# Kernel optimization log

Hardware: AMD Instinct MI355X
Metric: run time of the kernel (lower is better)

The kernel has to match this reference:

```python
import jax, jax.numpy as jnp
import numpy as np

BS, NC, C, D = 8, 64, 256, 32
K, KB, ALPHA, B = 16, 8, 4, 16
HS, HM, HMOD = 64, 64, 32
N = NC * C
DLM = NC * D
MOD_IN = K + 3 * D + 1    # 113
MOD_OUT = K + KB + 1 + D  # 57


def setup_inputs() -> dict:
    key = jax.random.key(0)
    ks = jax.random.split(key, 12)
    rn = lambda k, s, sc=1.0: jax.random.normal(k, s, dtype=jnp.float32) * sc
    s_in, m_in = 3 * D + 1, 3 * D
    inp = {}
    inp['cc_signals_t'] = rn(ks[0], (BS, DLM))
    inp['h'] = rn(ks[1], (BS, NC, C, D), 0.1)
    inp['prev_messages'] = rn(ks[2], (BS, NC, C, D), 0.1)
    inp['decay_logit'] = jnp.zeros((BS, NC, C), jnp.float32)
    inp['primitives_state'] = jnp.zeros((BS, NC, C, D), jnp.float32)
    inp['hebbian_traces'] = jnp.zeros((BS, NC, C, K), jnp.float32)
    inp['state_w1'] = rn(ks[3], (HS, s_in), (2.0 / (s_in + HS)) ** 0.5)
    inp['state_b1'] = jnp.zeros((HS,), jnp.float32)
    inp['state_w2'] = rn(ks[4], (D, HS), (2.0 / (HS + D)) ** 0.5)
    inp['state_b2'] = jnp.zeros((D,), jnp.float32)
    inp['msg_w1'] = rn(ks[5], (HM, m_in), (2.0 / (m_in + HM)) ** 0.5)
    inp['msg_b1'] = jnp.zeros((HM,), jnp.float32)
    inp['msg_w2'] = rn(ks[6], (D, HM), (2.0 / (HM + D)) ** 0.5)
    inp['msg_b2'] = jnp.zeros((D,), jnp.float32)
    inp['mod_w1'] = rn(ks[7], (N, HMOD, MOD_IN), (2.0 / (MOD_IN + HMOD)) ** 0.5)
    inp['mod_b1'] = jnp.zeros((N, HMOD), jnp.float32)
    inp['mod_w2'] = rn(ks[8], (N, HMOD, MOD_OUT), (2.0 / (HMOD + MOD_OUT)) ** 0.5)
    inp['mod_b2'] = jnp.zeros((N, MOD_OUT), jnp.float32)
    inp['neuron_id'] = rn(ks[9], (NC, C, D), 1.0 / D ** 0.5)
    inp['conn_indices'] = jax.random.randint(ks[10], (NC, C, K), 0, C)
    inp['border_conn_indices'] = jax.random.randint(ks[11], (NC, B, KB), 0, NC * B)
    return inp


def reference(cc_signals_t, h, prev_messages, decay_logit, primitives_state,
              hebbian_traces, state_w1, state_b1, state_w2, state_b2,
              msg_w1, msg_b1, msg_w2, msg_b2,
              mod_w1, mod_b1, mod_w2, mod_b2, neuron_id,
              conn_indices, border_conn_indices):
    # ---- per-neuron modulator: each of N=NC*C neurons has unique MLP weights ----
    nid = jnp.broadcast_to(neuron_id[None], (BS, NC, C, D))
    mod_inp = jnp.concatenate(
        [hebbian_traces, h, decay_logit[..., None], primitives_state, nid], axis=-1)
    flat = mod_inp.reshape(BS, N, MOD_IN)
    hid = jnp.tanh(jnp.einsum('bni,nhi->bnh', flat, mod_w1) + mod_b1)
    out = (jnp.einsum('bnh,nho->bno', hid, mod_w2) + mod_b2).reshape(BS, NC, C, MOD_OUT)
    new_w_conn = out[..., :K]                          # [BS,NC,C,K]
    w_border = out[:, :, ALPHA:ALPHA + B, K:K + KB]    # border neurons only [BS,NC,B,KB]
    new_decay = out[..., K + KB]                       # [BS,NC,C]
    new_prim = out[..., K + KB + 1:]                   # [BS,NC,C,D]

    # ---- intra-cell weighted neighbor gather (irregular gather) ----
    cell = jnp.arange(NC)[:, None, None]
    neighbor = prev_messages[:, cell, conn_indices]    # [BS,NC,C,K,D]
    received = jnp.einsum('bnckd,bnck->bncd', neighbor, jax.nn.sigmoid(new_w_conn))

    # ---- inter-cell border gather over global border neuron pool ----
    border_msgs = prev_messages[:, :, ALPHA:ALPHA + B, :].reshape(BS, NC * B, D)
    nb = border_msgs[:, border_conn_indices]           # [BS,NC,B,KB,D]
    recv_border = jnp.einsum('bnjkd,bnjk->bnjd', nb, jax.nn.sigmoid(w_border))
    received = received.at[:, :, ALPHA:ALPHA + B, :].add(recv_border)

    # ---- inject external signal into the first ALPHA neurons of each cell ----
    inj = cc_signals_t.reshape(BS, NC, 1, D)
    received = received.at[:, :, :ALPHA, :].add(
        jnp.broadcast_to(inj, (BS, NC, ALPHA, D)))

    # ---- decay-gated state update through shared state MLP ----
    primitives_new = primitives_state + new_prim
    decay = jax.nn.sigmoid(new_decay)[..., None]       # [BS,NC,C,1]
    s_in = jnp.concatenate([h, received, primitives_new, decay], axis=-1)  # 3D+1
    sh = jnp.tanh(jnp.einsum('...i,hi->...h', s_in, state_w1) + state_b1)
    dh = jnp.einsum('...h,dh->...d', sh, state_w2) + state_b2
    h_new = decay * h + (1.0 - decay) * jnp.tanh(dh)

    # ---- shared message MLP ----
    m_in = jnp.concatenate([h_new, received, nid], axis=-1)  # 3D
    mh = jnp.tanh(jnp.einsum('...i,hi->...h', m_in, msg_w1) + msg_b1)
    msg = jnp.tanh(jnp.einsum('...h,dh->...d', mh, msg_w2) + msg_b2)

    # ---- hebbian trace EMA: pre/post message correlation per connection ----
    nb_new = msg[:, cell, conn_indices]                # [BS,NC,C,K,D]
    corr = jnp.einsum('bncd,bnckd->bnck', msg, nb_new) / D
    hebbian_new = 0.9 * hebbian_traces + 0.1 * corr

    # ---- readout: mean over last ALPHA (readout) neurons per cell ----
    readout = msg[:, :, C - ALPHA:, :].mean(axis=2).reshape(BS, DLM)
    return readout, h_new, msg, hebbian_new
```

## Files before the change

### kernel.cpp

```cpp
#include <hip/hip_runtime.h>
#include <cstdint>
#include <cstddef>

constexpr int kBS = 8;
constexpr int kNC = 64;
constexpr int kC = 256;
constexpr int kD = 32;
constexpr int kK = 16;
constexpr int kKB = 8;
constexpr int kALPHA = 4;
constexpr int kB = 16;
constexpr int kHS = 64;
constexpr int kHM = 64;
constexpr int kHMOD = 32;
constexpr int kN = kNC * kC;
constexpr int kMODIN = kK + 3 * kD + 1;
constexpr int kMODOUT = kK + kKB + 1 + kD;
constexpr int kXS = 116;
constexpr int kW1S = 100;
constexpr int kSLAB = 36;

constexpr size_t kO1 = (size_t)kBS * kNC * kD;
constexpr size_t kO2 = kO1 + (size_t)kBS * kN * kD;
constexpr size_t kO3 = kO2 + (size_t)kBS * kN * kD;

__device__ __forceinline__ float sigmoidf_(float x) {
    return 1.0f / (1.0f + __expf(-x));
}
__device__ __forceinline__ float rdlane(float v, int l) {
    return __int_as_float(__builtin_amdgcn_readlane(__float_as_int(v), l));
}

__global__ __launch_bounds__(256) void mod_mlp_kernel(
    const float* __restrict__ heb, const float* __restrict__ h,
    const float* __restrict__ dlog, const float* __restrict__ prim,
    const float* __restrict__ nid,
    const float* __restrict__ mw1, const float* __restrict__ mb1,
    const float* __restrict__ mw2, const float* __restrict__ mb2,
    float* __restrict__ modout, int mos, int poff)
{
    const int wv = threadIdx.x >> 6;
    const int lane = threadIdx.x & 63;
    const int n = (blockIdx.x << 2) | wv;

    __shared__ __align__(16) float xs[4][kBS * kXS];
    float* xw = xs[wv];

    for (int t = lane; t < kBS * kMODIN; t += 64) {
        int b = t / kMODIN;
        int i = t - b * kMODIN;
        size_t nb = (size_t)b * kN + n;
        float v;
        if (i < kK)                 v = heb[nb * kK + i];
        else if (i < kK + kD)       v = h[nb * kD + (i - kK)];
        else if (i == kK + kD)      v = dlog[nb];
        else if (i < kK + 2*kD + 1) v = prim[nb * kD + (i - (kK + kD + 1))];
        else                        v = nid[(size_t)n * kD + (i - (kK + 2*kD + 1))];
        xw[b * kXS + i] = v;
    }
    __syncthreads();

    const int hh = lane & 31;
    const int bh = lane >> 5;
    const float* wg = mw1 + ((size_t)n * kHMOD + hh) * kMODIN;
    float a0 = 0.f, a1 = 0.f, a2 = 0.f, a3 = 0.f;
    #pragma unroll 4
    for (int q = 0; q < 28; ++q) {
        float w0 = wg[4*q+0], w1 = wg[4*q+1], w2 = wg[4*q+2], w3 = wg[4*q+3];
        const float4 x0 = *(const float4*)(xw + (bh+0) * kXS + 4*q);
        const float4 x1 = *(const float4*)(xw + (bh+2) * kXS + 4*q);
        const float4 x2 = *(const float4*)(xw + (bh+4) * kXS + 4*q);
        const float4 x3 = *(const float4*)(xw + (bh+6) * kXS + 4*q);
        a0 += w0*x0.x + w1*x0.y + w2*x0.z + w3*x0.w;
        a1 += w0*x1.x + w1*x1.y + w2*x1.z + w3*x1.w;
        a2 += w0*x2.x + w1*x2.y + w2*x2.z + w3*x2.w;
        a3 += w0*x3.x + w1*x3.y + w2*x3.z + w3*x3.w;
    }
    {
        float w112 = wg[112];
        a0 += w112 * xw[(bh+0)*kXS + 112];
        a1 += w112 * xw[(bh+2)*kXS + 112];
        a2 += w112 * xw[(bh+4)*kXS + 112];
        a3 += w112 * xw[(bh+6)*kXS + 112];
    }
    const float bb = mb1[(size_t)n * kHMOD + hh];
    float h0 = tanhf(a0 + bb);
    float h1 = tanhf(a1 + bb);
    float h2 = tanhf(a2 + bb);
    float h3 = tanhf(a3 + bb);

    const int o = (lane < kMODOUT) ? lane : (kMODOUT - 1);
    const float* w2g = mw2 + (size_t)n * (kHMOD * kMODOUT);
    float ob0=0.f, ob1=0.f, ob2=0.f, ob3=0.f, ob4=0.f, ob5=0.f, ob6=0.f, ob7=0.f;
    #pragma unroll
    for (int hx = 0; hx < kHMOD; ++hx) {
        float w = w2g[hx * kMODOUT + o];
        ob0 += rdlane(h0, hx)      * w;
        ob1 += rdlane(h0, hx + 32) * w;
        ob2 += rdlane(h1, hx)      * w;
        ob3 += rdlane(h1, hx + 32) * w;
        ob4 += rdlane(h2, hx)      * w;
        ob5 += rdlane(h2, hx + 32) * w;
        ob6 += rdlane(h3, hx)      * w;
        ob7 += rdlane(h3, hx + 32) * w;
    }
    if (lane < kMODOUT) {
        const float bo = mb2[(size_t)n * kMODOUT + o];
        const int oo = (o < 25) ? o : (o + (poff - 25));
        modout[((size_t)0 * kN + n) * mos + oo] = ob0 + bo;
        modout[((size_t)1 * kN + n) * mos + oo] = ob1 + bo;
        modout[((size_t)2 * kN + n) * mos + oo] = ob2 + bo;
        modout[((size_t)3 * kN + n) * mos + oo] = ob3 + bo;
        modout[((size_t)4 * kN + n) * mos + oo] = ob4 + bo;
        modout[((size_t)5 * kN + n) * mos + oo] = ob5 + bo;
        modout[((size_t)6 * kN + n) * mos + oo] = ob6 + bo;
        modout[((size_t)7 * kN + n) * mos + oo] = ob7 + bo;
    }
}

__global__ __launch_bounds__(256) void cell_kernel(
    const float* __restrict__ cc, const float* __restrict__ hin,
    const float* __restrict__ pmsg, const float* __restrict__ prim,
    const float* __restrict__ hebin, const float* __restrict__ nid,
    const float* __restrict__ sw1, const float* __restrict__ sb1,
    const float* __restrict__ sw2, const float* __restrict__ sb2,
    const float* __restrict__ mw1g, const float* __restrict__ mb1g,
    const float* __restrict__ mw2g, const float* __restrict__ mb2g,
    const int* __restrict__ conn, const int* __restrict__ bconn,
    const float* __restrict__ modout, float* __restrict__ out,
    int mos, int poff)
{
    const int nc = blockIdx.x;
    const int b  = blockIdx.y;
    const int c  = threadIdx.x;

    __shared__ __align__(16) float slab[kC * kSLAB];
    __shared__ __align__(16) float w1s[kHS * kW1S];
    __shared__ __align__(16) float w2ts[kHS * kD];
    __shared__ __align__(16) float mw1s[kHM * 96];
    __shared__ __align__(16) float mw2ts[kHM * kD];
    __shared__ float sb1s[kHS], sb2s[kD], mb1s[kHM], mb2s[kD];

    const size_t cellrow = ((size_t)b * kNC + nc) * kC;
    const size_t nbase   = cellrow + c;

    for (int idx = c; idx < kHS * 97; idx += kC) {
        int r = idx / 97, ci = idx - r * 97;
        w1s[r * kW1S + ci] = sw1[idx];
    }
    for (int idx = c; idx < kHM * 96; idx += kC) mw1s[idx] = mw1g[idx];
    for (int idx = c; idx < kHS * kD; idx += kC) {
        int o2 = idx >> 6, h2 = idx & 63;
        w2ts[h2 * kD + o2] = sw2[idx];
    }
    for (int idx = c; idx < kHM * kD; idx += kC) {
        int o2 = idx >> 6, h2 = idx & 63;
        mw2ts[h2 * kD + o2] = mw2g[idx];
    }
    if (c < kHS) sb1s[c] = sb1[c];
    if (c < kD)  sb2s[c] = sb2[c];
    if (c < kHM) mb1s[c] = mb1g[c];
    if (c < kD)  mb2s[c] = mb2g[c];

    {
        const float4* s4 = (const float4*)(pmsg + cellrow * kD);
        for (int i = c; i < (kC * kD) / 4; i += kC) {
            float4 v = s4[i];
            *(float4*)&slab[(i >> 3) * kSLAB + ((i & 7) << 2)] = v;
        }
    }

    float hreg[32];
    {
        const float4* src = (const float4*)(hin + nbase * kD);
        #pragma unroll
        for (int q = 0; q < 8; ++q) {
            float4 v = src[q];
            hreg[4*q] = v.x; hreg[4*q+1] = v.y; hreg[4*q+2] = v.z; hreg[4*q+3] = v.w;
        }
    }
    const float* mo = modout + nbase * mos;
    float wcon[16];
    if (poff == 28) {
        const float4* m4 = (const float4*)mo;
        float4 va = m4[0], vb = m4[1], vc = m4[2], vd = m4[3];
        wcon[0]=sigmoidf_(va.x);  wcon[1]=sigmoidf_(va.y);  wcon[2]=sigmoidf_(va.z);  wcon[3]=sigmoidf_(va.w);
        wcon[4]=sigmoidf_(vb.x);  wcon[5]=sigmoidf_(vb.y);  wcon[6]=sigmoidf_(vb.z);  wcon[7]=sigmoidf_(vb.w);
        wcon[8]=sigmoidf_(vc.x);  wcon[9]=sigmoidf_(vc.y);  wcon[10]=sigmoidf_(vc.z); wcon[11]=sigmoidf_(vc.w);
        wcon[12]=sigmoidf_(vd.x); wcon[13]=sigmoidf_(vd.y); wcon[14]=sigmoidf_(vd.z); wcon[15]=sigmoidf_(vd.w);
    } else {
        #pragma unroll
        for (int k = 0; k < 16; ++k) wcon[k] = sigmoidf_(mo[k]);
    }
    int jreg[16];
    {
        const int4* cr = (const int4*)(conn + ((size_t)nc * kC + c) * kK);
        #pragma unroll
        for (int q = 0; q < 4; ++q) {
            int4 v = cr[q];
            jreg[4*q] = v.x; jreg[4*q+1] = v.y; jreg[4*q+2] = v.z; jreg[4*q+3] = v.w;
        }
    }
    const float decay = sigmoidf_(mo[kK + kKB]);
    float pnew[32];
    {
        const float4* p4 = (const float4*)(prim + nbase * kD);
        if (poff == 28) {
            const float4* d4 = (const float4*)(mo + 28);
            #pragma unroll
            for (int q = 0; q < 8; ++q) {
                float4 v = p4[q], w = d4[q];
                pnew[4*q]   = v.x + w.x;
                pnew[4*q+1] = v.y + w.y;
                pnew[4*q+2] = v.z + w.z;
                pnew[4*q+3] = v.w + w.w;
            }
        } else {
            #pragma unroll
            for (int q = 0; q < 8; ++q) {
                float4 v = p4[q];
                pnew[4*q]   = v.x + mo[25 + 4*q];
                pnew[4*q+1] = v.y + mo[25 + 4*q + 1];
                pnew[4*q+2] = v.z + mo[25 + 4*q + 2];
                pnew[4*q+3] = v.w + mo[25 + 4*q + 3];
            }
        }
    }
    __syncthreads();

    float recv[32];
    #pragma unroll
    for (int d = 0; d < 32; ++d) recv[d] = 0.f;
    #pragma unroll 1
    for (int k = 0; k < 16; ++k) {
        const float4* row = (const float4*)(slab + jreg[k] * kSLAB);
        const float w = wcon[k];
        #pragma unroll
        for (int q = 0; q < 8; ++q) {
            float4 v = row[q];
            recv[4*q]   += v.x * w;
            recv[4*q+1] += v.y * w;
            recv[4*q+2] += v.z * w;
            recv[4*q+3] += v.w * w;
        }
    }
    if (c >= kALPHA && c < kALPHA + kB) {
        const int j = c - kALPHA;
        const int* br = bconn + ((size_t)nc * kB + j) * kKB;
        #pragma unroll 1
        for (int kb = 0; kb < kKB; ++kb) {
            int g = br[kb];
            int nc2 = g >> 4;
            int c2 = kALPHA + (g & 15);
            const float4* src = (const float4*)(pmsg + (((size_t)b * kNC + nc2) * kC + c2) * kD);
            float w = sigmoidf_(mo[kK + kb]);
            #pragma unroll
            for (int q = 0; q < 8; ++q) {
                float4 v = src[q];
                recv[4*q]   += v.x * w;
                recv[4*q+1] += v.y * w;
                recv[4*q+2] += v.z * w;
                recv[4*q+3] += v.w * w;
            }
        }
    }
    if (c < kALPHA) {
        const float* src = cc + (size_t)b * (kNC * kD) + nc * kD;
        #pragma unroll
        for (int d = 0; d < 32; ++d) recv[d] += src[d];
    }

    float dh[32];
    #pragma unroll
    for (int o = 0; o < 32; ++o) dh[o] = sb2s[o];
    #pragma unroll 2
    for (int hh = 0; hh < kHS; ++hh) {
        const float4* w4 = (const float4*)(w1s + hh * kW1S);
        float p0 = 0.f, p1 = 0.f, p2 = 0.f, p3 = 0.f;
        #pragma unroll
        for (int q = 0; q < 8; ++q) {
            float4 wv = w4[q];
            p0 += hreg[4*q] * wv.x;   p1 += hreg[4*q+1] * wv.y;
            p2 += hreg[4*q+2] * wv.z; p3 += hreg[4*q+3] * wv.w;
        }
        #pragma unroll
        for (int q = 0; q < 8; ++q) {
            float4 wv = w4[8+q];
            p0 += recv[4*q] * wv.x;   p1 += recv[4*q+1] * wv.y;
            p2 += recv[4*q+2] * wv.z; p3 += recv[4*q+3] * wv.w;
        }
        #pragma unroll
        for (int q = 0; q < 8; ++q) {
            float4 wv = w4[16+q];
            p0 += pnew[4*q] * wv.x;   p1 += pnew[4*q+1] * wv.y;
            p2 += pnew[4*q+2] * wv.z; p3 += pnew[4*q+3] * wv.w;
        }
        float acc = sb1s[hh] + ((p0 + p1) + (p2 + p3)) + decay * w1s[hh * kW1S + 96];
        const float s = tanhf(acc);
        const float4* w2r = (const float4*)(w2ts + hh * kD);
        #pragma unroll
        for (int q = 0; q < 8; ++q) {
            float4 wv = w2r[q];
            dh[4*q]   += s * wv.x;
            dh[4*q+1] += s * wv.y;
            dh[4*q+2] += s * wv.z;
            dh[4*q+3] += s * wv.w;
        }
    }
    float hnew[32];
    #pragma unroll
    for (int d = 0; d < 32; ++d) hnew[d] = decay * hreg[d] + (1.f - decay) * tanhf(dh[d]);

    {
        float4* dst = (float4*)(out + kO1 + nbase * kD);
        #pragma unroll
        for (int q = 0; q < 8; ++q)
            dst[q] = make_float4(hnew[4*q], hnew[4*q+1], hnew[4*q+2], hnew[4*q+3]);
    }

    float nidr[32];
    {
        const float4* src = (const float4*)(nid + ((size_t)nc * kC + c) * kD);
        #pragma unroll
        for (int q = 0; q < 8; ++q) {
            float4 v = src[q];
            nidr[4*q] = v.x; nidr[4*q+1] = v.y; nidr[4*q+2] = v.z; nidr[4*q+3] = v.w;
        }
    }
    float mm[32];
    #pragma unroll
    for (int o = 0; o < 32; ++o) mm[o] = mb2s[o];
    #pragma unroll 2
    for (int hh = 0; hh < kHM; ++hh) {
        const float4* w4 = (const float4*)(mw1s + hh * 96);
        float p0 = 0.f, p1 = 0.f, p2 = 0.f, p3 = 0.f;
        #pragma unroll
        for (int q = 0; q < 8; ++q) {
            float4 wv = w4[q];
            p0 += hnew[4*q] * wv.x;   p1 += hnew[4*q+1] * wv.y;
            p2 += hnew[4*q+2] * wv.z; p3 += hnew[4*q+3] * wv.w;
        }
        #pragma unroll
        for (int q = 0; q < 8; ++q) {
            float4 wv = w4[8+q];
            p0 += recv[4*q] * wv.x;   p1 += recv[4*q+1] * wv.y;
            p2 += recv[4*q+2] * wv.z; p3 += recv[4*q+3] * wv.w;
        }
        #pragma unroll
        for (int q = 0; q < 8; ++q) {
            float4 wv = w4[16+q];
            p0 += nidr[4*q] * wv.x;   p1 += nidr[4*q+1] * wv.y;
            p2 += nidr[4*q+2] * wv.z; p3 += nidr[4*q+3] * wv.w;
        }
        const float s = tanhf(mb1s[hh] + ((p0 + p1) + (p2 + p3)));
        const float4* w2r = (const float4*)(mw2ts + hh * kD);
        #pragma unroll
        for (int q = 0; q < 8; ++q) {
            float4 wv = w2r[q];
            mm[4*q]   += s * wv.x;
            mm[4*q+1] += s * wv.y;
            mm[4*q+2] += s * wv.z;
            mm[4*q+3] += s * wv.w;
        }
    }
    float msgr[32];
    #pragma unroll
    for (int d = 0; d < 32; ++d) msgr[d] = tanhf(mm[d]);

    __syncthreads();
    {
        float4* row = (float4*)(slab + c * kSLAB);
        #pragma unroll
        for (int q = 0; q < 8; ++q)
            row[q] = make_float4(msgr[4*q], msgr[4*q+1], msgr[4*q+2], msgr[4*q+3]);
    }
    __syncthreads();

    {
        const float* hb = hebin + nbase * kK;
        float* dst = out + kO3 + nbase * kK;
        #pragma unroll 1
        for (int k = 0; k < 16; ++k) {
            const float4* row = (const float4*)(slab + jreg[k] * kSLAB);
            float dot = 0.f;
            #pragma unroll
            for (int q = 0; q < 8; ++q) {
                float4 v = row[q];
                dot += msgr[4*q] * v.x + msgr[4*q+1] * v.y
                     + msgr[4*q+2] * v.z + msgr[4*q+3] * v.w;
            }
            dst[k] = 0.9f * hb[k] + 0.1f * (dot * (1.0f / 32.0f));
        }
    }
    {
        float4* dst = (float4*)(out + kO2 + cellrow * kD);
        for (int i = c; i < (kC * kD) / 4; i += kC)
            dst[i] = *(const float4*)&slab[(i >> 3) * kSLAB + ((i & 7) << 2)];
    }
    if (c < kD) {
        float s = 0.25f * (slab[(kC-4)*kSLAB + c] + slab[(kC-3)*kSLAB + c] +
                           slab[(kC-2)*kSLAB + c] + slab[(kC-1)*kSLAB + c]);
        out[(size_t)b * (kNC * kD) + nc * kD + c] = s;
    }
}

extern "C" void kernel_launch(void* const* d_in, const int* in_sizes, int n_in,
                              void* d_out, int out_size, void* d_ws, size_t ws_size,
                              hipStream_t stream)
{
    const float* cc    = (const float*)d_in[0];
    const float* h     = (const float*)d_in[1];
    const float* pmsg  = (const float*)d_in[2];
    const float* dlog  = (const float*)d_in[3];
    const float* prim  = (const float*)d_in[4];
    const float* heb   = (const float*)d_in[5];
    const float* sw1   = (const float*)d_in[6];
    const float* sb1   = (const float*)d_in[7];
    const float* sw2   = (const float*)d_in[8];
    const float* sb2   = (const float*)d_in[9];
    const float* mw1   = (const float*)d_in[10];
    const float* mb1   = (const float*)d_in[11];
    const float* mw2   = (const float*)d_in[12];
    const float* mb2   = (const float*)d_in[13];
    const float* modw1 = (const float*)d_in[14];
    const float* modb1 = (const float*)d_in[15];
    const float* modw2 = (const float*)d_in[16];
    const float* modb2 = (const float*)d_in[17];
    const float* nid   = (const float*)d_in[18];
    const int*   conn  = (const int*)d_in[19];
    const int*   bconn = (const int*)d_in[20];
    float* out = (float*)d_out;
    float* modout = (float*)d_ws;

    int mos = 57, poff = 25;
    if (ws_size >= (size_t)kBS * kN * 60 * sizeof(float)) { mos = 60; poff = 28; }

    mod_mlp_kernel<<<kN / 4, 256, 0, stream>>>(heb, h, dlog, prim, nid,
                                               modw1, modb1, modw2, modb2,
                                               modout, mos, poff);
    cell_kernel<<<dim3(kNC, kBS), kC, 0, stream>>>(cc, h, pmsg, prim, heb, nid,
                                                   sw1, sb1, sw2, sb2,
                                                   mw1, mb1, mw2, mb2,
                                                   conn, bconn, modout, out,
                                                   mos, poff);
}
```

Baseline: 766.1 us.

## Stage per-neuron modulator weights in LDS and pack two cells per cell-kernel block

The modulator kernel now loads each neuron's first-layer weight matrix with coalesced float4 reads into a padded LDS tile. The dot-product loop then reads float4 weight rows from LDS instead of strided scalar global loads. The per-wave __syncthreads is removed, since each wave reads only its own LDS region. The cell kernel now runs two cells per 512-thread block so the shared MLP weights are loaded once per pair of cells, at the cost of more LDS per block and changed occupancy.

```diff
diff --git a/kernel.cpp b/kernel.cpp
--- a/kernel.cpp
+++ b/kernel.cpp
@@ -17,6 +17,7 @@
 constexpr int kMODIN = kK + 3 * kD + 1;
 constexpr int kMODOUT = kK + kKB + 1 + kD;
 constexpr int kXS = 116;
+constexpr int kWS = 116;
 constexpr int kW1S = 100;
 constexpr int kSLAB = 36;
 
@@ -44,7 +45,25 @@
     const int n = (blockIdx.x << 2) | wv;
 
     __shared__ __align__(16) float xs[4][kBS * kXS];
-    float* xw = xs[wv];
+    __shared__ __align__(16) float w1sh[4][kHMOD * kWS];
+    float* xw  = xs[wv];
+    float* w1s = w1sh[wv];
+
+    {
+        const float4* w1g4 = (const float4*)(mw1 + (size_t)n * (kHMOD * kMODIN));
+        for (int t = lane; t < (kHMOD * kMODIN) / 4; t += 64) {
+            float4 v = w1g4[t];
+            int f = t << 2;
+            #pragma unroll
+            for (int e = 0; e < 4; ++e) {
+                int fe = f + e;
+                int r = fe / kMODIN;
+                int col = fe - r * kMODIN;
+                float val = (e == 0) ? v.x : (e == 1) ? v.y : (e == 2) ? v.z : v.w;
+                w1s[r * kWS + col] = val;
+            }
+        }
+    }
 
     for (int t = lane; t < kBS * kMODIN; t += 64) {
         int b = t / kMODIN;
@@ -58,26 +77,25 @@
         else                        v = nid[(size_t)n * kD + (i - (kK + 2*kD + 1))];
         xw[b * kXS + i] = v;
     }
-    __syncthreads();
 
     const int hh = lane & 31;
     const int bh = lane >> 5;
-    const float* wg = mw1 + ((size_t)n * kHMOD + hh) * kMODIN;
+    const float* wr = w1s + hh * kWS;
     float a0 = 0.f, a1 = 0.f, a2 = 0.f, a3 = 0.f;
     #pragma unroll 4
     for (int q = 0; q < 28; ++q) {
-        float w0 = wg[4*q+0], w1 = wg[4*q+1], w2 = wg[4*q+2], w3 = wg[4*q+3];
+        const float4 wv4 = *(const float4*)(wr + 4*q);
         const float4 x0 = *(const float4*)(xw + (bh+0) * kXS + 4*q);
         const float4 x1 = *(const float4*)(xw + (bh+2) * kXS + 4*q);
         const float4 x2 = *(const float4*)(xw + (bh+4) * kXS + 4*q);
         const float4 x3 = *(const float4*)(xw + (bh+6) * kXS + 4*q);
-        a0 += w0*x0.x + w1*x0.y + w2*x0.z + w3*x0.w;
-        a1 += w0*x1.x + w1*x1.y + w2*x1.z + w3*x1.w;
-        a2 += w0*x2.x + w1*x2.y + w2*x2.z + w3*x2.w;
-        a3 += w0*x3.x + w1*x3.y + w2*x3.z + w3*x3.w;
-    }
-    {
-        float w112 = wg[112];
+        a0 += wv4.x*x0.x + wv4.y*x0.y + wv4.z*x0.z + wv4.w*x0.w;
+        a1 += wv4.x*x1.x + wv4.y*x1.y + wv4.z*x1.z + wv4.w*x1.w;
+        a2 += wv4.x*x2.x + wv4.y*x2.y + wv4.z*x2.z + wv4.w*x2.w;
+        a3 += wv4.x*x3.x + wv4.y*x3.y + wv4.z*x3.z + wv4.w*x3.w;
+    }
+    {
+        float w112 = wr[112];
         a0 += w112 * xw[(bh+0)*kXS + 112];
         a1 += w112 * xw[(bh+2)*kXS + 112];
         a2 += w112 * xw[(bh+4)*kXS + 112];
@@ -118,7 +136,7 @@
     }
 }
 
-__global__ __launch_bounds__(256) void cell_kernel(
+__global__ __launch_bounds__(512, 2) void cell_kernel(
     const float* __restrict__ cc, const float* __restrict__ hin,
     const float* __restrict__ pmsg, const float* __restrict__ prim,
     const float* __restrict__ hebin, const float* __restrict__ nid,
@@ -130,37 +148,39 @@
     const float* __restrict__ modout, float* __restrict__ out,
     int mos, int poff)
 {
-    const int nc = blockIdx.x;
-    const int b  = blockIdx.y;
-    const int c  = threadIdx.x;
-
-    __shared__ __align__(16) float slab[kC * kSLAB];
+    const int half = threadIdx.x >> 8;
+    const int c    = threadIdx.x & 255;
+    const int nc   = (blockIdx.x << 1) | half;
+    const int b    = blockIdx.y;
+
+    __shared__ __align__(16) float slab2[2][kC * kSLAB];
     __shared__ __align__(16) float w1s[kHS * kW1S];
     __shared__ __align__(16) float w2ts[kHS * kD];
     __shared__ __align__(16) float mw1s[kHM * 96];
     __shared__ __align__(16) float mw2ts[kHM * kD];
     __shared__ float sb1s[kHS], sb2s[kD], mb1s[kHM], mb2s[kD];
 
+    float* slab = slab2[half];
     const size_t cellrow = ((size_t)b * kNC + nc) * kC;
     const size_t nbase   = cellrow + c;
 
-    for (int idx = c; idx < kHS * 97; idx += kC) {
+    for (int idx = threadIdx.x; idx < kHS * 97; idx += 512) {
         int r = idx / 97, ci = idx - r * 97;
         w1s[r * kW1S + ci] = sw1[idx];
     }
-    for (int idx = c; idx < kHM * 96; idx += kC) mw1s[idx] = mw1g[idx];
-    for (int idx = c; idx < kHS * kD; idx += kC) {
+    for (int idx = threadIdx.x; idx < kHM * 96; idx += 512) mw1s[idx] = mw1g[idx];
+    for (int idx = threadIdx.x; idx < kHS * kD; idx += 512) {
         int o2 = idx >> 6, h2 = idx & 63;
         w2ts[h2 * kD + o2] = sw2[idx];
     }
-    for (int idx = c; idx < kHM * kD; idx += kC) {
+    for (int idx = threadIdx.x; idx < kHM * kD; idx += 512) {
         int o2 = idx >> 6, h2 = idx & 63;
         mw2ts[h2 * kD + o2] = mw2g[idx];
     }
-    if (c < kHS) sb1s[c] = sb1[c];
-    if (c < kD)  sb2s[c] = sb2[c];
-    if (c < kHM) mb1s[c] = mb1g[c];
-    if (c < kD)  mb2s[c] = mb2g[c];
+    if (threadIdx.x < kHS)  sb1s[threadIdx.x] = sb1[threadIdx.x];
+    if (threadIdx.x < kD)   sb2s[threadIdx.x] = sb2[threadIdx.x];
+    if (threadIdx.x >= 64 && threadIdx.x < 64 + kHM) mb1s[threadIdx.x - 64] = mb1g[threadIdx.x - 64];
+    if (threadIdx.x >= 128 && threadIdx.x < 128 + kD) mb2s[threadIdx.x - 128] = mb2g[threadIdx.x - 128];
 
     {
         const float4* s4 = (const float4*)(pmsg + cellrow * kD);
@@ -438,9 +458,9 @@
     mod_mlp_kernel<<<kN / 4, 256, 0, stream>>>(heb, h, dlog, prim, nid,
                                                modw1, modb1, modw2, modb2,
                                                modout, mos, poff);
-    cell_kernel<<<dim3(kNC, kBS), kC, 0, stream>>>(cc, h, pmsg, prim, heb, nid,
-                                                   sw1, sb1, sw2, sb2,
-                                                   mw1, mb1, mw2, mb2,
-                                                   conn, bconn, modout, out,
-                                                   mos, poff);
+    cell_kernel<<<dim3(kNC / 2, kBS), 512, 0, stream>>>(cc, h, pmsg, prim, heb, nid,
+                                                        sw1, sb1, sw2, sb2,
+                                                        mw1, mb1, mw2, mb2,
+                                                        conn, bconn, modout, out,
+                                                        mos, poff);
 }
```

After: 756.2 us. About the same (-1.3%).
